# Optimization experiments

Hardware: AMD Instinct MI355X
Metric: run time of the kernel (lower is better)

The kernel has to match this reference:

```python
import jax, jax.numpy as jnp
import numpy as np

N_NODES = 50000
N_EDGES = 800000
N_GRAPHS = 512
F_IN = 128
H = 64


def setup_inputs() -> dict:
    key = jax.random.key(0)
    ks = jax.random.split(key, 12)
    x = jax.random.normal(ks[0], (N_NODES, F_IN), dtype=jnp.float32)
    edge_index = jax.random.randint(ks[1], (2, N_EDGES), 0, N_NODES, dtype=jnp.int64)
    batch = jnp.sort(jax.random.randint(ks[2], (N_NODES,), 0, N_GRAPHS, dtype=jnp.int64))
    def glorot(k, shape):
        lim = float(np.sqrt(6.0 / (shape[0] + shape[1])))
        return jax.random.uniform(k, shape, jnp.float32, -lim, lim)
    return {
        "x": x,
        "edge_index": edge_index,
        "batch": batch,
        "W1": glorot(ks[3], (F_IN, H)), "b1": jnp.zeros((H,), jnp.float32),
        "W2": glorot(ks[4], (H, H)),    "b2": jnp.zeros((H,), jnp.float32),
        "Wf1": glorot(ks[5], (H, 128)), "bf1": jnp.zeros((128,), jnp.float32),
        "Wf2": glorot(ks[6], (128, 1)), "bf2": jnp.zeros((1,), jnp.float32),
    }


def gcn_conv(x, src, dst, norm, W, b):
    # x' = D^{-1/2}(A+I)D^{-1/2} (x W) + b   (self-loops already in src/dst)
    xw = x @ W                                   # [N, H]
    msgs = xw[src] * norm[:, None]               # gather + scale, [E+N, H]
    agg = jax.ops.segment_sum(msgs, dst, num_segments=N_NODES)  # scatter-add
    return agg + b


def reference(x, edge_index, batch, W1, b1, W2, b2, Wf1, bf1, Wf2, bf2):
    loops = jnp.arange(N_NODES, dtype=edge_index.dtype)
    src = jnp.concatenate([edge_index[0], loops])
    dst = jnp.concatenate([edge_index[1], loops])
    # symmetric normalization: deg computed with self-loops, counted at dst
    deg = jax.ops.segment_sum(jnp.ones_like(dst, dtype=x.dtype), dst, num_segments=N_NODES)
    dinv = jax.lax.rsqrt(jnp.maximum(deg, 1.0))
    norm = dinv[src] * dinv[dst]

    h = jax.nn.relu(gcn_conv(x, src, dst, norm, W1, b1))
    h = jax.nn.relu(gcn_conv(h, src, dst, norm, W2, b2))

    # global mean pool over graphs
    sums = jax.ops.segment_sum(h, batch, num_segments=N_GRAPHS)      # [G, H]
    cnts = jax.ops.segment_sum(jnp.ones((N_NODES,), h.dtype), batch, num_segments=N_GRAPHS)
    pooled = sums / jnp.maximum(cnts, 1.0)[:, None]

    out = jax.nn.relu(pooled @ Wf1 + bf1)
    out = out @ Wf2 + bf2
    return out.squeeze(-1)
```

## Files before the change

### kernel.cpp

```cpp
#include <hip/hip_runtime.h>
#include <hip/hip_fp16.h>

#define N_NODES 50000
#define N_EDGES 800000
#define N_GRAPHS 512
#define F_IN 128
#define HDIM 64
#define NBUCK 196
#define BCAP 5120
#define EPB 4096
#define N_P1 ((N_EDGES + EPB - 1) / EPB)
#define MAXPER 20

typedef _Float16 half8 __attribute__((ext_vector_type(8)));
typedef float f32x4 __attribute__((ext_vector_type(4)));

__global__ __launch_bounds__(256) void twt_k(const float* __restrict__ W1, const float* __restrict__ W2,
                                             _Float16* __restrict__ Wt1, _Float16* __restrict__ Wt2,
                                             int* __restrict__ bTot) {
    int t = threadIdx.x;
    bTot[t] = 0;
    for (int m = t; m < F_IN * HDIM; m += 256) { int k = m >> 6, c = m & 63; Wt1[c * F_IN + k] = (_Float16)W1[m]; }
    for (int m = t; m < HDIM * HDIM; m += 256) { int k = m >> 6, c = m & 63; Wt2[c * HDIM + k] = (_Float16)W2[m]; }
}

__global__ __launch_bounds__(256) void pass1_k(const int* __restrict__ src, const int* __restrict__ dst,
                                               int* __restrict__ bucketTot, int* __restrict__ stage) {
    __shared__ int cnt[256];
    __shared__ int pf[256];
    __shared__ int goff[256];
    __shared__ int lpk[EPB];
    __shared__ unsigned char bkn[EPB];
    int t = threadIdx.x;
    cnt[t] = 0;
    __syncthreads();
    int base = blockIdx.x * EPB + t * 16;
    int packed[16], bk[16], rk[16];
    bool full = (blockIdx.x + 1) * EPB <= N_EDGES;
    if (full) {
        const int4* s4 = (const int4*)(src + base);
        const int4* d4 = (const int4*)(dst + base);
        #pragma unroll
        for (int q = 0; q < 4; ++q) {
            int4 sv = s4[q], dv = d4[q];
            int ss[4] = {sv.x, sv.y, sv.z, sv.w};
            int dd[4] = {dv.x, dv.y, dv.z, dv.w};
            #pragma unroll
            for (int j = 0; j < 4; ++j) {
                int b = dd[j] >> 8;
                rk[q * 4 + j] = atomicAdd(&cnt[b], 1);
                bk[q * 4 + j] = b;
                packed[q * 4 + j] = ss[j] | ((dd[j] & 255) << 16);
            }
        }
    } else {
        #pragma unroll
        for (int k = 0; k < 16; ++k) {
            int e = base + k;
            if (e < N_EDGES) {
                int d = dst[e];
                int b = d >> 8;
                rk[k] = atomicAdd(&cnt[b], 1);
                bk[k] = b;
                packed[k] = src[e] | ((d & 255) << 16);
            } else bk[k] = -1;
        }
    }
    __syncthreads();
    int cv = cnt[t];
    pf[t] = cv; __syncthreads();
    for (int off = 1; off < 256; off <<= 1) {
        int u = (t >= off) ? pf[t - off] : 0; __syncthreads();
        pf[t] += u; __syncthreads();
    }
    if (cv > 0) goff[t] = atomicAdd(&bucketTot[t], cv);
    #pragma unroll
    for (int k = 0; k < 16; ++k) {
        if (bk[k] >= 0) {
            int b = bk[k];
            int p = pf[b] - cnt[b] + rk[k];
            lpk[p] = packed[k];
            bkn[p] = (unsigned char)b;
        }
    }
    __syncthreads();
    int tot = pf[255];
    for (int i = t; i < tot; i += 256) {
        int b = bkn[i];
        int local = i - (pf[b] - cnt[b]);
        stage[b * BCAP + goff[b] + local] = lpk[i];
    }
}

__global__ __launch_bounds__(256) void pass2_k(const int* __restrict__ stage, const int* __restrict__ bucketTot,
                                               int* __restrict__ row, float* __restrict__ dinv,
                                               int* __restrict__ csr) {
    __shared__ int cnt[256];
    __shared__ int pf[256];
    __shared__ int sb[256];
    __shared__ int lcsr[BCAP];
    int b = blockIdx.x, t = threadIdx.x;
    int tot = bucketTot[b];
    int v = (t < NBUCK) ? bucketTot[t] : 0;
    sb[t] = v; __syncthreads();
    for (int off = 1; off < 256; off <<= 1) {
        int u = (t >= off) ? sb[t - off] : 0; __syncthreads();
        sb[t] += u; __syncthreads();
    }
    int base = sb[b] - tot;
    if (b == 0 && t == 0) row[N_NODES] = N_EDGES;
    cnt[t] = 0; __syncthreads();
    int myp[MAXPER], myr[MAXPER];
    #pragma unroll
    for (int k = 0; k < MAXPER; ++k) {
        int i = t + k * 256;
        if (i < tot) {
            int p = stage[b * BCAP + i];
            int loc = (p >> 16) & 255;
            myp[k] = p;
            myr[k] = atomicAdd(&cnt[loc], 1);
        } else myp[k] = -1;
    }
    __syncthreads();
    int cv = cnt[t];
    pf[t] = cv; __syncthreads();
    for (int off = 1; off < 256; off <<= 1) {
        int u = (t >= off) ? pf[t - off] : 0; __syncthreads();
        pf[t] += u; __syncthreads();
    }
    int node = b * 256 + t;
    if (node < N_NODES) {
        row[node] = base + pf[t] - cv;
        dinv[node] = rsqrtf((float)cv + 1.0f);
    }
    #pragma unroll
    for (int k = 0; k < MAXPER; ++k) {
        if (myp[k] >= 0) {
            int loc = (myp[k] >> 16) & 255;
            lcsr[pf[loc] - cnt[loc] + myr[k]] = myp[k] & 0xFFFF;
        }
    }
    __syncthreads();
    for (int i = t; i < tot; i += 256) csr[base + i] = lcsr[i];
}

__global__ __launch_bounds__(256) void xw1_k(const float* __restrict__ x, const _Float16* __restrict__ Wt1,
                                             const float* __restrict__ dinv, _Float16* __restrict__ xwh) {
    __shared__ _Float16 xs[64][136];
    __shared__ _Float16 wt[64][136];
    __shared__ _Float16 outt[64][72];
    int t = threadIdx.x;
    int row0 = blockIdx.x * 64;
    const float4* x4 = (const float4*)x;
    #pragma unroll
    for (int i = 0; i < 8; ++i) {
        int m = t + i * 256;
        int n = m >> 5, k4 = m & 31;
        int gn = row0 + n;
        float4 v = make_float4(0.f, 0.f, 0.f, 0.f);
        if (gn < N_NODES) v = x4[gn * 32 + k4];
        _Float16* p = &xs[n][k4 * 4];
        p[0] = (_Float16)v.x; p[1] = (_Float16)v.y; p[2] = (_Float16)v.z; p[3] = (_Float16)v.w;
    }
    const uint4* wt4 = (const uint4*)Wt1;
    #pragma unroll
    for (int i = 0; i < 4; ++i) {
        int m = t + i * 256;
        int c = m >> 4, k8 = m & 15;
        *(uint4*)&wt[c][k8 * 8] = wt4[m];
    }
    __syncthreads();
    int w = t >> 6, lane = t & 63, r = lane & 15, q = lane >> 4;
    half8 a[4];
    #pragma unroll
    for (int kk = 0; kk < 4; ++kk) a[kk] = *(const half8*)&xs[w * 16 + r][kk * 32 + q * 8];
    float dv[4];
    #pragma unroll
    for (int reg = 0; reg < 4; ++reg) {
        int n = row0 + w * 16 + q * 4 + reg;
        dv[reg] = (n < N_NODES) ? dinv[n] : 0.f;
    }
    #pragma unroll
    for (int ct = 0; ct < 4; ++ct) {
        f32x4 acc = {0.f, 0.f, 0.f, 0.f};
        #pragma unroll
        for (int kk = 0; kk < 4; ++kk) {
            half8 b = *(const half8*)&wt[ct * 16 + r][kk * 32 + q * 8];
            acc = __builtin_amdgcn_mfma_f32_16x16x32_f16(a[kk], b, acc, 0, 0, 0);
        }
        #pragma unroll
        for (int reg = 0; reg < 4; ++reg)
            outt[w * 16 + q * 4 + reg][ct * 16 + r] = (_Float16)(acc[reg] * dv[reg]);
    }
    __syncthreads();
    #pragma unroll
    for (int i = 0; i < 2; ++i) {
        int m = t + i * 256;
        int n = m >> 3, c8 = m & 7;
        int gn = row0 + n;
        if (gn < N_NODES) {
            uint4 v = *(const uint4*)&outt[n][c8 * 8];
            ((uint4*)xwh)[gn * 8 + c8] = v;
        }
    }
}

__global__ __launch_bounds__(256) void conv2_k(const _Float16* __restrict__ h1, const _Float16* __restrict__ Wt2,
                                               const float* __restrict__ dinv, _Float16* __restrict__ xwh) {
    __shared__ _Float16 hs[64][72];
    __shared__ _Float16 wt[64][72];
    __shared__ _Float16 outt[64][72];
    int t = threadIdx.x;
    int row0 = blockIdx.x * 64;
    const uint4* h8 = (const uint4*)h1;
    #pragma unroll
    for (int i = 0; i < 2; ++i) {
        int m = t + i * 256;
        int n = m >> 3, k8 = m & 7;
        int gn = row0 + n;
        uint4 v = make_uint4(0u, 0u, 0u, 0u);
        if (gn < N_NODES) v = h8[gn * 8 + k8];
        *(uint4*)&hs[n][k8 * 8] = v;
    }
    const uint4* wt4 = (const uint4*)Wt2;
    #pragma unroll
    for (int i = 0; i < 2; ++i) {
        int m = t + i * 256;
        int c = m >> 3, k8 = m & 7;
        *(uint4*)&wt[c][k8 * 8] = wt4[m];
    }
    __syncthreads();
    int w = t >> 6, lane = t & 63, r = lane & 15, q = lane >> 4;
    half8 a0 = *(const half8*)&hs[w * 16 + r][q * 8];
    half8 a1 = *(const half8*)&hs[w * 16 + r][32 + q * 8];
    float dv[4];
    #pragma unroll
    for (int reg = 0; reg < 4; ++reg) {
        int n = row0 + w * 16 + q * 4 + reg;
        dv[reg] = (n < N_NODES) ? dinv[n] : 0.f;
    }
    #pragma unroll
    for (int ct = 0; ct < 4; ++ct) {
        f32x4 acc = {0.f, 0.f, 0.f, 0.f};
        half8 b0 = *(const half8*)&wt[ct * 16 + r][q * 8];
        half8 b1 = *(const half8*)&wt[ct * 16 + r][32 + q * 8];
        acc = __builtin_amdgcn_mfma_f32_16x16x32_f16(a0, b0, acc, 0, 0, 0);
        acc = __builtin_amdgcn_mfma_f32_16x16x32_f16(a1, b1, acc, 0, 0, 0);
        #pragma unroll
        for (int reg = 0; reg < 4; ++reg)
            outt[w * 16 + q * 4 + reg][ct * 16 + r] = (_Float16)(acc[reg] * dv[reg]);
    }
    __syncthreads();
    #pragma unroll
    for (int i = 0; i < 2; ++i) {
        int m = t + i * 256;
        int n = m >> 3, c8 = m & 7;
        int gn = row0 + n;
        if (gn < N_NODES) {
            uint4 v = *(const uint4*)&outt[n][c8 * 8];
            ((uint4*)xwh)[gn * 8 + c8] = v;
        }
    }
}

__device__ inline void acc8(uint4 v, float* a) {
    float2 f;
    f = __half22float2(__builtin_bit_cast(__half2, v.x)); a[0] += f.x; a[1] += f.y;
    f = __half22float2(__builtin_bit_cast(__half2, v.y)); a[2] += f.x; a[3] += f.y;
    f = __half22float2(__builtin_bit_cast(__half2, v.z)); a[4] += f.x; a[5] += f.y;
    f = __half22float2(__builtin_bit_cast(__half2, v.w)); a[6] += f.x; a[7] += f.y;
}

__global__ __launch_bounds__(256) void gather_k(const _Float16* __restrict__ xwh, const int* __restrict__ row,
                                                const int* __restrict__ csr, const float* __restrict__ dinv,
                                                const float* __restrict__ bias, _Float16* __restrict__ hout) {
    int t = threadIdx.x;
    int node = blockIdx.x * 4 + (t >> 6);
    int lane = t & 63;
    int fq = lane & 7, eslot = lane >> 3;
    const uint4* xw4 = (const uint4*)xwh;
    float a[8];
    #pragma unroll
    for (int k = 0; k < 8; ++k) a[k] = 0.f;
    if (eslot == 0) acc8(xw4[node * 8 + fq], a);
    int j = row[node] + eslot, jend = row[node + 1];
    for (; j + 8 < jend; j += 16) {
        int s0 = csr[j], s1 = csr[j + 8];
        uint4 v0 = xw4[s0 * 8 + fq];
        uint4 v1 = xw4[s1 * 8 + fq];
        acc8(v0, a); acc8(v1, a);
    }
    if (j < jend) acc8(xw4[csr[j] * 8 + fq], a);
    #pragma unroll
    for (int k = 0; k < 8; ++k) {
        a[k] += __shfl_xor(a[k], 8);
        a[k] += __shfl_xor(a[k], 16);
        a[k] += __shfl_xor(a[k], 32);
    }
    if (eslot == 0) {
        float dd = dinv[node];
        const float4* b4 = (const float4*)bias;
        float4 bl = b4[fq * 2], bh = b4[fq * 2 + 1];
        float r0 = fmaxf(a[0] * dd + bl.x, 0.f), r1 = fmaxf(a[1] * dd + bl.y, 0.f);
        float r2 = fmaxf(a[2] * dd + bl.z, 0.f), r3 = fmaxf(a[3] * dd + bl.w, 0.f);
        float r4 = fmaxf(a[4] * dd + bh.x, 0.f), r5 = fmaxf(a[5] * dd + bh.y, 0.f);
        float r6 = fmaxf(a[6] * dd + bh.z, 0.f), r7 = fmaxf(a[7] * dd + bh.w, 0.f);
        __half2 p0 = __float22half2_rn(make_float2(r0, r1));
        __half2 p1 = __float22half2_rn(make_float2(r2, r3));
        __half2 p2 = __float22half2_rn(make_float2(r4, r5));
        __half2 p3 = __float22half2_rn(make_float2(r6, r7));
        uint4 o;
        o.x = __builtin_bit_cast(unsigned int, p0);
        o.y = __builtin_bit_cast(unsigned int, p1);
        o.z = __builtin_bit_cast(unsigned int, p2);
        o.w = __builtin_bit_cast(unsigned int, p3);
        ((uint4*)hout)[node * 8 + fq] = o;
    }
}

__device__ inline int lower_bound_i(const int* __restrict__ a, int n, int v) {
    int lo = 0, hi = n;
    while (lo < hi) { int m = (lo + hi) >> 1; if (a[m] < v) lo = m + 1; else hi = m; }
    return lo;
}

__global__ __launch_bounds__(256) void pool_k(const _Float16* __restrict__ h, const int* __restrict__ batch,
                                              float* __restrict__ pooled) {
    __shared__ int se[2];
    __shared__ float red[4][64];
    int g = blockIdx.x, t = threadIdx.x;
    if (t == 0) { se[0] = lower_bound_i(batch, N_NODES, g); se[1] = lower_bound_i(batch, N_NODES, g + 1); }
    __syncthreads();
    int start = se[0], end = se[1];
    int w = t >> 6, lane = t & 63;
    float acc = 0.f;
    for (int n = start + w; n < end; n += 4) acc += (float)h[n * 64 + lane];
    red[w][lane] = acc; __syncthreads();
    if (w == 0) {
        float v = red[0][lane] + red[1][lane] + red[2][lane] + red[3][lane];
        int c = end - start;
        pooled[g * 64 + lane] = v / (float)max(c, 1);
    }
}

__global__ __launch_bounds__(128) void mlp_k(const float* __restrict__ pooled,
                                             const float* __restrict__ Wf1, const float* __restrict__ bf1,
                                             const float* __restrict__ Wf2, const float* __restrict__ bf2,
                                             float* __restrict__ out) {
    __shared__ float ps[HDIM];
    __shared__ float wsum[2];
    int g = blockIdx.x, t = threadIdx.x;
    if (t < HDIM) ps[t] = pooled[g * HDIM + t];
    __syncthreads();
    float acc = bf1[t];
    #pragma unroll 8
    for (int k = 0; k < HDIM; ++k) acc += ps[k] * Wf1[k * 128 + t];
    acc = fmaxf(acc, 0.f) * Wf2[t];
    #pragma unroll
    for (int off = 32; off > 0; off >>= 1) acc += __shfl_down(acc, off);
    if ((t & 63) == 0) wsum[t >> 6] = acc;
    __syncthreads();
    if (t == 0) out[g] = wsum[0] + wsum[1] + bf2[0];
}

extern "C" void kernel_launch(void* const* d_in, const int* in_sizes, int n_in,
                              void* d_out, int out_size, void* d_ws, size_t ws_size,
                              hipStream_t stream) {
    const float* x    = (const float*)d_in[0];
    const int*   ei   = (const int*)d_in[1];
    const int*   src  = ei;
    const int*   dst  = ei + N_EDGES;
    const int*   batch= (const int*)d_in[2];
    const float* W1   = (const float*)d_in[3];
    const float* b1   = (const float*)d_in[4];
    const float* W2   = (const float*)d_in[5];
    const float* b2   = (const float*)d_in[6];
    const float* Wf1  = (const float*)d_in[7];
    const float* bf1  = (const float*)d_in[8];
    const float* Wf2  = (const float*)d_in[9];
    const float* bf2  = (const float*)d_in[10];
    float* out = (float*)d_out;

    char* p = (char*)d_ws;
    _Float16* xwh  = (_Float16*)p;  p += (size_t)N_NODES * HDIM * 2;
    _Float16* h1b  = (_Float16*)p;  p += (size_t)N_NODES * HDIM * 2;
    _Float16* h2b  = (_Float16*)p;  p += (size_t)N_NODES * HDIM * 2;
    _Float16* Wt1  = (_Float16*)p;  p += (size_t)F_IN * HDIM * 2;
    _Float16* Wt2  = (_Float16*)p;  p += (size_t)HDIM * HDIM * 2;
    float*  dinv   = (float*)p;     p += (size_t)N_NODES * 4;
    float*  pooled = (float*)p;     p += (size_t)N_GRAPHS * HDIM * 4;
    int*    row    = (int*)p;       p += (size_t)(N_NODES + 1) * 4;
    int*    csr    = (int*)p;       p += (size_t)N_EDGES * 4;
    int*    bTot   = (int*)p;       p += 256 * 4;
    int*    stage  = (int*)p;       p += (size_t)NBUCK * BCAP * 4;

    twt_k<<<1, 256, 0, stream>>>(W1, W2, Wt1, Wt2, bTot);
    pass1_k<<<N_P1, 256, 0, stream>>>(src, dst, bTot, stage);
    pass2_k<<<NBUCK, 256, 0, stream>>>(stage, bTot, row, dinv, csr);

    xw1_k<<<(N_NODES + 63) / 64, 256, 0, stream>>>(x, Wt1, dinv, xwh);
    gather_k<<<N_NODES / 4, 256, 0, stream>>>(xwh, row, csr, dinv, b1, h1b);
    conv2_k<<<(N_NODES + 63) / 64, 256, 0, stream>>>(h1b, Wt2, dinv, xwh);
    gather_k<<<N_NODES / 4, 256, 0, stream>>>(xwh, row, csr, dinv, b2, h2b);

    pool_k<<<N_GRAPHS, 256, 0, stream>>>(h2b, batch, pooled);
    mlp_k<<<N_GRAPHS, 128, 0, stream>>>(pooled, Wf1, bf1, Wf2, bf2, out);
}
```

Before: 206.7 us.

## Use finer CSR buckets, prefetch gather indices, fuse pooling with MLP

```diff
diff --git a/kernel.cpp b/kernel.cpp
--- a/kernel.cpp
+++ b/kernel.cpp
@@ -6,11 +6,13 @@
 #define N_GRAPHS 512
 #define F_IN 128
 #define HDIM 64
-#define NBUCK 196
-#define BCAP 5120
-#define EPB 4096
+#define BSH 7
+#define NBUCK 391
+#define BCAP 2560
+#define EPB 2048
 #define N_P1 ((N_EDGES + EPB - 1) / EPB)
-#define MAXPER 20
+#define MAXPER 10
+#define EMAX (N_EDGES - 1)
 
 typedef _Float16 half8 __attribute__((ext_vector_type(8)));
 typedef float f32x4 __attribute__((ext_vector_type(4)));
@@ -19,75 +21,81 @@
                                              _Float16* __restrict__ Wt1, _Float16* __restrict__ Wt2,
                                              int* __restrict__ bTot) {
     int t = threadIdx.x;
-    bTot[t] = 0;
+    bTot[t] = 0; bTot[t + 256] = 0;
     for (int m = t; m < F_IN * HDIM; m += 256) { int k = m >> 6, c = m & 63; Wt1[c * F_IN + k] = (_Float16)W1[m]; }
     for (int m = t; m < HDIM * HDIM; m += 256) { int k = m >> 6, c = m & 63; Wt2[c * HDIM + k] = (_Float16)W2[m]; }
 }
 
 __global__ __launch_bounds__(256) void pass1_k(const int* __restrict__ src, const int* __restrict__ dst,
                                                int* __restrict__ bucketTot, int* __restrict__ stage) {
-    __shared__ int cnt[256];
-    __shared__ int pf[256];
-    __shared__ int goff[256];
+    __shared__ int cnt[512];
+    __shared__ int pfE[512];
+    __shared__ int sb[256];
+    __shared__ int goff[512];
     __shared__ int lpk[EPB];
-    __shared__ unsigned char bkn[EPB];
+    __shared__ unsigned short bkn[EPB];
     int t = threadIdx.x;
-    cnt[t] = 0;
-    __syncthreads();
-    int base = blockIdx.x * EPB + t * 16;
-    int packed[16], bk[16], rk[16];
+    cnt[t] = 0; cnt[t + 256] = 0;
+    __syncthreads();
+    int base = blockIdx.x * EPB + t * 8;
+    int packed[8], bk[8], rk[8];
     bool full = (blockIdx.x + 1) * EPB <= N_EDGES;
     if (full) {
         const int4* s4 = (const int4*)(src + base);
         const int4* d4 = (const int4*)(dst + base);
         #pragma unroll
-        for (int q = 0; q < 4; ++q) {
+        for (int q = 0; q < 2; ++q) {
             int4 sv = s4[q], dv = d4[q];
             int ss[4] = {sv.x, sv.y, sv.z, sv.w};
             int dd[4] = {dv.x, dv.y, dv.z, dv.w};
             #pragma unroll
-            for (int j = 0; j < 4; ++j) {
-                int b = dd[j] >> 8;
-                rk[q * 4 + j] = atomicAdd(&cnt[b], 1);
-                bk[q * 4 + j] = b;
-                packed[q * 4 + j] = ss[j] | ((dd[j] & 255) << 16);
+            for (int jj = 0; jj < 4; ++jj) {
+                int b = dd[jj] >> BSH;
+                rk[q * 4 + jj] = atomicAdd(&cnt[b], 1);
+                bk[q * 4 + jj] = b;
+                packed[q * 4 + jj] = ss[jj] | ((dd[jj] & 127) << 16);
             }
         }
     } else {
         #pragma unroll
-        for (int k = 0; k < 16; ++k) {
+        for (int k = 0; k < 8; ++k) {
             int e = base + k;
             if (e < N_EDGES) {
                 int d = dst[e];
-                int b = d >> 8;
+                int b = d >> BSH;
                 rk[k] = atomicAdd(&cnt[b], 1);
                 bk[k] = b;
-                packed[k] = src[e] | ((d & 255) << 16);
+                packed[k] = src[e] | ((d & 127) << 16);
             } else bk[k] = -1;
         }
     }
     __syncthreads();
-    int cv = cnt[t];
-    pf[t] = cv; __syncthreads();
+    int c0 = cnt[2 * t], c1 = cnt[2 * t + 1];
+    int ps = c0 + c1;
+    sb[t] = ps; __syncthreads();
     for (int off = 1; off < 256; off <<= 1) {
-        int u = (t >= off) ? pf[t - off] : 0; __syncthreads();
-        pf[t] += u; __syncthreads();
-    }
-    if (cv > 0) goff[t] = atomicAdd(&bucketTot[t], cv);
-    #pragma unroll
-    for (int k = 0; k < 16; ++k) {
+        int u = (t >= off) ? sb[t - off] : 0; __syncthreads();
+        sb[t] += u; __syncthreads();
+    }
+    int bp = sb[t] - ps;
+    pfE[2 * t] = bp; pfE[2 * t + 1] = bp + c0;
+    if (c0 > 0) goff[2 * t] = atomicAdd(&bucketTot[2 * t], c0);
+    if (c1 > 0) goff[2 * t + 1] = atomicAdd(&bucketTot[2 * t + 1], c1);
+    __syncthreads();
+    #pragma unroll
+    for (int k = 0; k < 8; ++k) {
         if (bk[k] >= 0) {
             int b = bk[k];
-            int p = pf[b] - cnt[b] + rk[k];
+            int p = pfE[b] + rk[k];
             lpk[p] = packed[k];
-            bkn[p] = (unsigned char)b;
-        }
-    }
-    __syncthreads();
-    int tot = pf[255];
+            bkn[p] = (unsigned short)b;
+        }
+    }
+    __syncthreads();
+    int tot = sb[255];
     for (int i = t; i < tot; i += 256) {
         int b = bkn[i];
-        int local = i - (pf[b] - cnt[b]);
+        int local = i - pfE[b];
         stage[b * BCAP + goff[b] + local] = lpk[i];
     }
 }
@@ -98,16 +106,21 @@
     __shared__ int cnt[256];
     __shared__ int pf[256];
     __shared__ int sb[256];
+    __shared__ int sbE[512];
     __shared__ int lcsr[BCAP];
     int b = blockIdx.x, t = threadIdx.x;
     int tot = bucketTot[b];
-    int v = (t < NBUCK) ? bucketTot[t] : 0;
-    sb[t] = v; __syncthreads();
+    int c0 = bucketTot[2 * t], c1 = bucketTot[2 * t + 1];
+    int ps = c0 + c1;
+    sb[t] = ps; __syncthreads();
     for (int off = 1; off < 256; off <<= 1) {
         int u = (t >= off) ? sb[t - off] : 0; __syncthreads();
         sb[t] += u; __syncthreads();
     }
-    int base = sb[b] - tot;
+    int bp = sb[t] - ps;
+    sbE[2 * t] = bp; sbE[2 * t + 1] = bp + c0;
+    __syncthreads();
+    int base = sbE[b];
     if (b == 0 && t == 0) row[N_NODES] = N_EDGES;
     cnt[t] = 0; __syncthreads();
     int myp[MAXPER], myr[MAXPER];
@@ -128,8 +141,8 @@
         int u = (t >= off) ? pf[t - off] : 0; __syncthreads();
         pf[t] += u; __syncthreads();
     }
-    int node = b * 256 + t;
-    if (node < N_NODES) {
+    int node = (b << BSH) + t;
+    if (t < 128 && node < N_NODES) {
         row[node] = base + pf[t] - cv;
         dinv[node] = rsqrtf((float)cv + 1.0f);
     }
@@ -284,13 +297,16 @@
     for (int k = 0; k < 8; ++k) a[k] = 0.f;
     if (eslot == 0) acc8(xw4[node * 8 + fq], a);
     int j = row[node] + eslot, jend = row[node + 1];
+    int s0 = csr[min(j, EMAX)];
+    int s1 = csr[min(j + 8, EMAX)];
     for (; j + 8 < jend; j += 16) {
-        int s0 = csr[j], s1 = csr[j + 8];
         uint4 v0 = xw4[s0 * 8 + fq];
         uint4 v1 = xw4[s1 * 8 + fq];
+        s0 = csr[min(j + 16, EMAX)];
+        s1 = csr[min(j + 24, EMAX)];
         acc8(v0, a); acc8(v1, a);
     }
-    if (j < jend) acc8(xw4[csr[j] * 8 + fq], a);
+    if (j < jend) acc8(xw4[s0 * 8 + fq], a);
     #pragma unroll
     for (int k = 0; k < 8; ++k) {
         a[k] += __shfl_xor(a[k], 8);
@@ -324,10 +340,14 @@
     return lo;
 }
 
-__global__ __launch_bounds__(256) void pool_k(const _Float16* __restrict__ h, const int* __restrict__ batch,
-                                              float* __restrict__ pooled) {
+__global__ __launch_bounds__(256) void poolmlp_k(const _Float16* __restrict__ h, const int* __restrict__ batch,
+                                                 const float* __restrict__ Wf1, const float* __restrict__ bf1,
+                                                 const float* __restrict__ Wf2, const float* __restrict__ bf2,
+                                                 float* __restrict__ out) {
     __shared__ int se[2];
     __shared__ float red[4][64];
+    __shared__ float ps[64];
+    __shared__ float wsum[2];
     int g = blockIdx.x, t = threadIdx.x;
     if (t == 0) { se[0] = lower_bound_i(batch, N_NODES, g); se[1] = lower_bound_i(batch, N_NODES, g + 1); }
     __syncthreads();
@@ -339,26 +359,20 @@
     if (w == 0) {
         float v = red[0][lane] + red[1][lane] + red[2][lane] + red[3][lane];
         int c = end - start;
-        pooled[g * 64 + lane] = v / (float)max(c, 1);
-    }
-}
-
-__global__ __launch_bounds__(128) void mlp_k(const float* __restrict__ pooled,
-                                             const float* __restrict__ Wf1, const float* __restrict__ bf1,
-                                             const float* __restrict__ Wf2, const float* __restrict__ bf2,
-                                             float* __restrict__ out) {
-    __shared__ float ps[HDIM];
-    __shared__ float wsum[2];
-    int g = blockIdx.x, t = threadIdx.x;
-    if (t < HDIM) ps[t] = pooled[g * HDIM + t];
-    __syncthreads();
-    float acc = bf1[t];
-    #pragma unroll 8
-    for (int k = 0; k < HDIM; ++k) acc += ps[k] * Wf1[k * 128 + t];
-    acc = fmaxf(acc, 0.f) * Wf2[t];
-    #pragma unroll
-    for (int off = 32; off > 0; off >>= 1) acc += __shfl_down(acc, off);
-    if ((t & 63) == 0) wsum[t >> 6] = acc;
+        ps[lane] = v / (float)max(c, 1);
+    }
+    __syncthreads();
+    float v = 0.f;
+    if (t < 128) {
+        float a2 = bf1[t];
+        #pragma unroll 8
+        for (int k = 0; k < HDIM; ++k) a2 += ps[k] * Wf1[k * 128 + t];
+        v = fmaxf(a2, 0.f) * Wf2[t];
+        #pragma unroll
+        for (int off = 32; off > 0; off >>= 1) v += __shfl_down(v, off);
+    }
+    if (t == 0) wsum[0] = v;
+    if (t == 64) wsum[1] = v;
     __syncthreads();
     if (t == 0) out[g] = wsum[0] + wsum[1] + bf2[0];
 }
@@ -388,10 +402,9 @@
     _Float16* Wt1  = (_Float16*)p;  p += (size_t)F_IN * HDIM * 2;
     _Float16* Wt2  = (_Float16*)p;  p += (size_t)HDIM * HDIM * 2;
     float*  dinv   = (float*)p;     p += (size_t)N_NODES * 4;
-    float*  pooled = (float*)p;     p += (size_t)N_GRAPHS * HDIM * 4;
     int*    row    = (int*)p;       p += (size_t)(N_NODES + 1) * 4;
     int*    csr    = (int*)p;       p += (size_t)N_EDGES * 4;
-    int*    bTot   = (int*)p;       p += 256 * 4;
+    int*    bTot   = (int*)p;       p += 512 * 4;
     int*    stage  = (int*)p;       p += (size_t)NBUCK * BCAP * 4;
 
     twt_k<<<1, 256, 0, stream>>>(W1, W2, Wt1, Wt2, bTot);
@@ -403,6 +416,5 @@
     conv2_k<<<(N_NODES + 63) / 64, 256, 0, stream>>>(h1b, Wt2, dinv, xwh);
     gather_k<<<N_NODES / 4, 256, 0, stream>>>(xwh, row, csr, dinv, b2, h2b);
 
-    pool_k<<<N_GRAPHS, 256, 0, stream>>>(h2b, batch, pooled);
-    mlp_k<<<N_GRAPHS, 128, 0, stream>>>(pooled, Wf1, bf1, Wf2, bf2, out);
-}
+    poolmlp_k<<<N_GRAPHS, 256, 0, stream>>>(h2b, batch, Wf1, bf1, Wf2, bf2, out);
+}
```

Result: slower. 211.7 us (+2.4%).

## Fuse second gather with mean pooling, compact CSR to u16, use wave scans

Applied to the files above, without the earlier changes.

```diff
diff --git a/kernel.cpp b/kernel.cpp
--- a/kernel.cpp
+++ b/kernel.cpp
@@ -15,20 +15,34 @@
 typedef _Float16 half8 __attribute__((ext_vector_type(8)));
 typedef float f32x4 __attribute__((ext_vector_type(4)));
 
-__global__ __launch_bounds__(256) void twt_k(const float* __restrict__ W1, const float* __restrict__ W2,
-                                             _Float16* __restrict__ Wt1, _Float16* __restrict__ Wt2,
-                                             int* __restrict__ bTot) {
-    int t = threadIdx.x;
-    bTot[t] = 0;
-    for (int m = t; m < F_IN * HDIM; m += 256) { int k = m >> 6, c = m & 63; Wt1[c * F_IN + k] = (_Float16)W1[m]; }
-    for (int m = t; m < HDIM * HDIM; m += 256) { int k = m >> 6, c = m & 63; Wt2[c * HDIM + k] = (_Float16)W2[m]; }
+__device__ inline int wave_incl_scan(int v, int lane) {
+    #pragma unroll
+    for (int off = 1; off < 64; off <<= 1) {
+        int u = __shfl_up(v, off);
+        if (lane >= off) v += u;
+    }
+    return v;
+}
+
+__global__ __launch_bounds__(256) void prep_k(const float* __restrict__ W1, const float* __restrict__ W2,
+                                              _Float16* __restrict__ Wt1, _Float16* __restrict__ Wt2,
+                                              int* __restrict__ bTot, float* __restrict__ pooled) {
+    int t = threadIdx.x;
+    int id = blockIdx.x * 256 + t;
+    if (blockIdx.x == 0) bTot[t] = 0;
+    pooled[id] = 0.f;
+    pooled[id + 16384] = 0.f;
+    if (id < F_IN * HDIM) { int k = id >> 6, c = id & 63; Wt1[c * F_IN + k] = (_Float16)W1[id]; }
+    if (id < HDIM * HDIM) { int k = id >> 6, c = id & 63; Wt2[c * HDIM + k] = (_Float16)W2[id]; }
 }
 
 __global__ __launch_bounds__(256) void pass1_k(const int* __restrict__ src, const int* __restrict__ dst,
                                                int* __restrict__ bucketTot, int* __restrict__ stage) {
     __shared__ int cnt[256];
-    __shared__ int pf[256];
+    __shared__ int pfE[256];
     __shared__ int goff[256];
+    __shared__ int wsum[4];
+    __shared__ int totS;
     __shared__ int lpk[EPB];
     __shared__ unsigned char bkn[EPB];
     int t = threadIdx.x;
@@ -46,11 +60,11 @@
             int ss[4] = {sv.x, sv.y, sv.z, sv.w};
             int dd[4] = {dv.x, dv.y, dv.z, dv.w};
             #pragma unroll
-            for (int j = 0; j < 4; ++j) {
-                int b = dd[j] >> 8;
-                rk[q * 4 + j] = atomicAdd(&cnt[b], 1);
-                bk[q * 4 + j] = b;
-                packed[q * 4 + j] = ss[j] | ((dd[j] & 255) << 16);
+            for (int jj = 0; jj < 4; ++jj) {
+                int b = dd[jj] >> 8;
+                rk[q * 4 + jj] = atomicAdd(&cnt[b], 1);
+                bk[q * 4 + jj] = b;
+                packed[q * 4 + jj] = ss[jj] | ((dd[jj] & 255) << 16);
             }
         }
     } else {
@@ -68,46 +82,63 @@
     }
     __syncthreads();
     int cv = cnt[t];
-    pf[t] = cv; __syncthreads();
-    for (int off = 1; off < 256; off <<= 1) {
-        int u = (t >= off) ? pf[t - off] : 0; __syncthreads();
-        pf[t] += u; __syncthreads();
-    }
+    int w = t >> 6, lane = t & 63;
+    int inc = wave_incl_scan(cv, lane);
+    if (lane == 63) wsum[w] = inc;
+    __syncthreads();
+    if (w == 0) {
+        int x = (lane < 4) ? wsum[lane] : 0;
+        x = wave_incl_scan(x, lane);
+        if (lane < 4) wsum[lane] = x;
+    }
+    __syncthreads();
+    int excl = inc - cv + ((w > 0) ? wsum[w - 1] : 0);
+    pfE[t] = excl;
+    if (t == 255) totS = excl + cv;
     if (cv > 0) goff[t] = atomicAdd(&bucketTot[t], cv);
+    __syncthreads();
     #pragma unroll
     for (int k = 0; k < 16; ++k) {
         if (bk[k] >= 0) {
             int b = bk[k];
-            int p = pf[b] - cnt[b] + rk[k];
+            int p = pfE[b] + rk[k];
             lpk[p] = packed[k];
             bkn[p] = (unsigned char)b;
         }
     }
     __syncthreads();
-    int tot = pf[255];
+    int tot = totS;
     for (int i = t; i < tot; i += 256) {
         int b = bkn[i];
-        int local = i - (pf[b] - cnt[b]);
+        int local = i - pfE[b];
         stage[b * BCAP + goff[b] + local] = lpk[i];
     }
 }
 
 __global__ __launch_bounds__(256) void pass2_k(const int* __restrict__ stage, const int* __restrict__ bucketTot,
                                                int* __restrict__ row, float* __restrict__ dinv,
-                                               int* __restrict__ csr) {
+                                               unsigned short* __restrict__ csr) {
     __shared__ int cnt[256];
     __shared__ int pf[256];
-    __shared__ int sb[256];
+    __shared__ int wsum[4];
+    __shared__ int baseS;
     __shared__ int lcsr[BCAP];
     int b = blockIdx.x, t = threadIdx.x;
     int tot = bucketTot[b];
-    int v = (t < NBUCK) ? bucketTot[t] : 0;
-    sb[t] = v; __syncthreads();
-    for (int off = 1; off < 256; off <<= 1) {
-        int u = (t >= off) ? sb[t - off] : 0; __syncthreads();
-        sb[t] += u; __syncthreads();
-    }
-    int base = sb[b] - tot;
+    int w = t >> 6, lane = t & 63;
+    {
+        int v = (t < NBUCK) ? bucketTot[t] : 0;
+        int inc = wave_incl_scan(v, lane);
+        if (lane == 63) wsum[w] = inc;
+        __syncthreads();
+        if (w == 0) {
+            int x = (lane < 4) ? wsum[lane] : 0;
+            x = wave_incl_scan(x, lane);
+            if (lane < 4) wsum[lane] = x;
+        }
+        __syncthreads();
+        if (t == b) baseS = inc - v + ((w > 0) ? wsum[w - 1] : 0);
+    }
     if (b == 0 && t == 0) row[N_NODES] = N_EDGES;
     cnt[t] = 0; __syncthreads();
     int myp[MAXPER], myr[MAXPER];
@@ -123,25 +154,33 @@
     }
     __syncthreads();
     int cv = cnt[t];
-    pf[t] = cv; __syncthreads();
-    for (int off = 1; off < 256; off <<= 1) {
-        int u = (t >= off) ? pf[t - off] : 0; __syncthreads();
-        pf[t] += u; __syncthreads();
-    }
-    int node = b * 256 + t;
+    int inc = wave_incl_scan(cv, lane);
+    if (lane == 63) wsum[w] = inc;
+    __syncthreads();
+    if (w == 0) {
+        int x = (lane < 4) ? wsum[lane] : 0;
+        x = wave_incl_scan(x, lane);
+        if (lane < 4) wsum[lane] = x;
+    }
+    __syncthreads();
+    int excl = inc - cv + ((w > 0) ? wsum[w - 1] : 0);
+    pf[t] = excl;
+    __syncthreads();
+    int base = baseS;
+    int node = (b << 8) + t;
     if (node < N_NODES) {
-        row[node] = base + pf[t] - cv;
+        row[node] = base + excl;
         dinv[node] = rsqrtf((float)cv + 1.0f);
     }
     #pragma unroll
     for (int k = 0; k < MAXPER; ++k) {
         if (myp[k] >= 0) {
             int loc = (myp[k] >> 16) & 255;
-            lcsr[pf[loc] - cnt[loc] + myr[k]] = myp[k] & 0xFFFF;
-        }
-    }
-    __syncthreads();
-    for (int i = t; i < tot; i += 256) csr[base + i] = lcsr[i];
+            lcsr[pf[loc] + myr[k]] = myp[k] & 0xFFFF;
+        }
+    }
+    __syncthreads();
+    for (int i = t; i < tot; i += 256) csr[base + i] = (unsigned short)lcsr[i];
 }
 
 __global__ __launch_bounds__(256) void xw1_k(const float* __restrict__ x, const _Float16* __restrict__ Wt1,
@@ -272,7 +311,7 @@
 }
 
 __global__ __launch_bounds__(256) void gather_k(const _Float16* __restrict__ xwh, const int* __restrict__ row,
-                                                const int* __restrict__ csr, const float* __restrict__ dinv,
+                                                const unsigned short* __restrict__ csr, const float* __restrict__ dinv,
                                                 const float* __restrict__ bias, _Float16* __restrict__ hout) {
     int t = threadIdx.x;
     int node = blockIdx.x * 4 + (t >> 6);
@@ -318,47 +357,90 @@
     }
 }
 
+__global__ __launch_bounds__(256) void gather2pool_k(const _Float16* __restrict__ xwh, const int* __restrict__ row,
+                                                     const unsigned short* __restrict__ csr, const float* __restrict__ dinv,
+                                                     const float* __restrict__ bias, const int* __restrict__ batch,
+                                                     float* __restrict__ pooled) {
+    __shared__ float hacc[4][64];
+    __shared__ int gid[4];
+    int t = threadIdx.x;
+    int wv = t >> 6;
+    int node = blockIdx.x * 4 + wv;
+    int lane = t & 63;
+    int fq = lane & 7, eslot = lane >> 3;
+    const uint4* xw4 = (const uint4*)xwh;
+    float a[8];
+    #pragma unroll
+    for (int k = 0; k < 8; ++k) a[k] = 0.f;
+    if (eslot == 0) acc8(xw4[node * 8 + fq], a);
+    int j = row[node] + eslot, jend = row[node + 1];
+    for (; j + 8 < jend; j += 16) {
+        int s0 = csr[j], s1 = csr[j + 8];
+        uint4 v0 = xw4[s0 * 8 + fq];
+        uint4 v1 = xw4[s1 * 8 + fq];
+        acc8(v0, a); acc8(v1, a);
+    }
+    if (j < jend) acc8(xw4[csr[j] * 8 + fq], a);
+    #pragma unroll
+    for (int k = 0; k < 8; ++k) {
+        a[k] += __shfl_xor(a[k], 8);
+        a[k] += __shfl_xor(a[k], 16);
+        a[k] += __shfl_xor(a[k], 32);
+    }
+    if (lane == 0) gid[wv] = batch[node];
+    if (eslot == 0) {
+        float dd = dinv[node];
+        const float4* b4 = (const float4*)bias;
+        float4 bl = b4[fq * 2], bh = b4[fq * 2 + 1];
+        hacc[wv][fq * 8 + 0] = fmaxf(a[0] * dd + bl.x, 0.f);
+        hacc[wv][fq * 8 + 1] = fmaxf(a[1] * dd + bl.y, 0.f);
+        hacc[wv][fq * 8 + 2] = fmaxf(a[2] * dd + bl.z, 0.f);
+        hacc[wv][fq * 8 + 3] = fmaxf(a[3] * dd + bl.w, 0.f);
+        hacc[wv][fq * 8 + 4] = fmaxf(a[4] * dd + bh.x, 0.f);
+        hacc[wv][fq * 8 + 5] = fmaxf(a[5] * dd + bh.y, 0.f);
+        hacc[wv][fq * 8 + 6] = fmaxf(a[6] * dd + bh.z, 0.f);
+        hacc[wv][fq * 8 + 7] = fmaxf(a[7] * dd + bh.w, 0.f);
+    }
+    __syncthreads();
+    if (t < 64) {
+        int g0 = gid[0];
+        if (gid[1] == g0 && gid[2] == g0 && gid[3] == g0) {
+            float s = hacc[0][t] + hacc[1][t] + hacc[2][t] + hacc[3][t];
+            atomicAdd(&pooled[g0 * 64 + t], s);
+        } else {
+            #pragma unroll
+            for (int w2 = 0; w2 < 4; ++w2) atomicAdd(&pooled[gid[w2] * 64 + t], hacc[w2][t]);
+        }
+    }
+}
+
 __device__ inline int lower_bound_i(const int* __restrict__ a, int n, int v) {
     int lo = 0, hi = n;
     while (lo < hi) { int m = (lo + hi) >> 1; if (a[m] < v) lo = m + 1; else hi = m; }
     return lo;
 }
 
-__global__ __launch_bounds__(256) void pool_k(const _Float16* __restrict__ h, const int* __restrict__ batch,
-                                              float* __restrict__ pooled) {
-    __shared__ int se[2];
-    __shared__ float red[4][64];
-    int g = blockIdx.x, t = threadIdx.x;
-    if (t == 0) { se[0] = lower_bound_i(batch, N_NODES, g); se[1] = lower_bound_i(batch, N_NODES, g + 1); }
-    __syncthreads();
-    int start = se[0], end = se[1];
-    int w = t >> 6, lane = t & 63;
-    float acc = 0.f;
-    for (int n = start + w; n < end; n += 4) acc += (float)h[n * 64 + lane];
-    red[w][lane] = acc; __syncthreads();
-    if (w == 0) {
-        float v = red[0][lane] + red[1][lane] + red[2][lane] + red[3][lane];
-        int c = end - start;
-        pooled[g * 64 + lane] = v / (float)max(c, 1);
-    }
-}
-
-__global__ __launch_bounds__(128) void mlp_k(const float* __restrict__ pooled,
+__global__ __launch_bounds__(128) void mlp_k(const float* __restrict__ pooled, const int* __restrict__ batch,
                                              const float* __restrict__ Wf1, const float* __restrict__ bf1,
                                              const float* __restrict__ Wf2, const float* __restrict__ bf2,
                                              float* __restrict__ out) {
-    __shared__ float ps[HDIM];
+    __shared__ int se[2];
+    __shared__ float ps[64];
     __shared__ float wsum[2];
     int g = blockIdx.x, t = threadIdx.x;
-    if (t < HDIM) ps[t] = pooled[g * HDIM + t];
-    __syncthreads();
-    float acc = bf1[t];
+    if (t == 0) { se[0] = lower_bound_i(batch, N_NODES, g); se[1] = lower_bound_i(batch, N_NODES, g + 1); }
+    __syncthreads();
+    int c = se[1] - se[0];
+    float inv = 1.0f / (float)max(c, 1);
+    if (t < 64) ps[t] = pooled[g * 64 + t] * inv;
+    __syncthreads();
+    float a2 = bf1[t];
     #pragma unroll 8
-    for (int k = 0; k < HDIM; ++k) acc += ps[k] * Wf1[k * 128 + t];
-    acc = fmaxf(acc, 0.f) * Wf2[t];
-    #pragma unroll
-    for (int off = 32; off > 0; off >>= 1) acc += __shfl_down(acc, off);
-    if ((t & 63) == 0) wsum[t >> 6] = acc;
+    for (int k = 0; k < HDIM; ++k) a2 += ps[k] * Wf1[k * 128 + t];
+    float v = fmaxf(a2, 0.f) * Wf2[t];
+    #pragma unroll
+    for (int off = 32; off > 0; off >>= 1) v += __shfl_down(v, off);
+    if ((t & 63) == 0) wsum[t >> 6] = v;
     __syncthreads();
     if (t == 0) out[g] = wsum[0] + wsum[1] + bf2[0];
 }
@@ -384,25 +466,23 @@
     char* p = (char*)d_ws;
     _Float16* xwh  = (_Float16*)p;  p += (size_t)N_NODES * HDIM * 2;
     _Float16* h1b  = (_Float16*)p;  p += (size_t)N_NODES * HDIM * 2;
-    _Float16* h2b  = (_Float16*)p;  p += (size_t)N_NODES * HDIM * 2;
     _Float16* Wt1  = (_Float16*)p;  p += (size_t)F_IN * HDIM * 2;
     _Float16* Wt2  = (_Float16*)p;  p += (size_t)HDIM * HDIM * 2;
     float*  dinv   = (float*)p;     p += (size_t)N_NODES * 4;
     float*  pooled = (float*)p;     p += (size_t)N_GRAPHS * HDIM * 4;
     int*    row    = (int*)p;       p += (size_t)(N_NODES + 1) * 4;
-    int*    csr    = (int*)p;       p += (size_t)N_EDGES * 4;
+    unsigned short* csr = (unsigned short*)p; p += (size_t)N_EDGES * 2;
     int*    bTot   = (int*)p;       p += 256 * 4;
     int*    stage  = (int*)p;       p += (size_t)NBUCK * BCAP * 4;
 
-    twt_k<<<1, 256, 0, stream>>>(W1, W2, Wt1, Wt2, bTot);
+    prep_k<<<64, 256, 0, stream>>>(W1, W2, Wt1, Wt2, bTot, pooled);
     pass1_k<<<N_P1, 256, 0, stream>>>(src, dst, bTot, stage);
     pass2_k<<<NBUCK, 256, 0, stream>>>(stage, bTot, row, dinv, csr);
 
     xw1_k<<<(N_NODES + 63) / 64, 256, 0, stream>>>(x, Wt1, dinv, xwh);
     gather_k<<<N_NODES / 4, 256, 0, stream>>>(xwh, row, csr, dinv, b1, h1b);
     conv2_k<<<(N_NODES + 63) / 64, 256, 0, stream>>>(h1b, Wt2, dinv, xwh);
-    gather_k<<<N_NODES / 4, 256, 0, stream>>>(xwh, row, csr, dinv, b2, h2b);
-
-    pool_k<<<N_GRAPHS, 256, 0, stream>>>(h2b, batch, pooled);
-    mlp_k<<<N_GRAPHS, 128, 0, stream>>>(pooled, Wf1, bf1, Wf2, bf2, out);
-}
+    gather2pool_k<<<N_NODES / 4, 256, 0, stream>>>(xwh, row, csr, dinv, b2, batch, pooled);
+
+    mlp_k<<<N_GRAPHS, 128, 0, stream>>>(pooled, batch, Wf1, bf1, Wf2, bf2, out);
+}
```

New measurement: 184.0 us. -11.0%, faster.
